# Kernel optimization log

Measured on AMD Instinct MI355X. Metric: run time of the kernel, lower is better.

Reference implementation:

```python
import jax, jax.numpy as jnp
import numpy as np

LN_EPS = 1e-5
NEG_INF = -1e38


def wkv_scan(w, u, k, v):
    """Numerically-stable RWKV WKV recurrence (matches wkv_cuda forward).
    w: [C] (negative decay), u: [C] bonus, k/v: [B,T,C]. Returns y: [B,T,C]."""
    Bdim, T, C = k.shape

    def step(carry, kv_t):
        p, q, o = carry  # running num, den, log-scale, each [B,C]
        kt, vt = kv_t
        no = jnp.maximum(o, u + kt)
        A = jnp.exp(o - no)
        Bw = jnp.exp(u + kt - no)
        y = (A * p + Bw * vt) / (A * q + Bw)
        no2 = jnp.maximum(w + o, kt)
        A2 = jnp.exp(w + o - no2)
        B2 = jnp.exp(kt - no2)
        return (A2 * p + B2 * vt, A2 * q + B2, no2), y

    init = (jnp.zeros((Bdim, C), k.dtype), jnp.zeros((Bdim, C), k.dtype),
            jnp.full((Bdim, C), NEG_INF, k.dtype))
    kT = jnp.moveaxis(k, 1, 0)  # [T,B,C]
    vT = jnp.moveaxis(v, 1, 0)
    _, ys = jax.lax.scan(step, init, (kT, vT))
    return jnp.moveaxis(ys, 0, 1)  # [B,T,C]


def setup_inputs() -> dict:
    key = jax.random.key(0)
    ks = jax.random.split(key, 8)
    B, C, H, W = 16, 192, 56, 56
    s = 0.02
    x = jax.random.normal(ks[0], (B, C, H, W), jnp.float32)
    Wk = jax.random.normal(ks[1], (C, C), jnp.float32) * s
    Wv = jax.random.normal(ks[2], (C, C), jnp.float32) * s
    Wr = jax.random.normal(ks[3], (C, C), jnp.float32) * s
    Wo = jax.random.normal(ks[4], (C, C), jnp.float32) * s
    ln_g = jnp.ones((C,), jnp.float32)
    ln_b = jnp.zeros((C,), jnp.float32)
    w_decay = -6.0 + 0.1 * jax.random.normal(ks[5], (C,), jnp.float32)
    u = 0.1 * jax.random.normal(ks[6], (C,), jnp.float32)
    return {"x": x, "Wk": Wk, "Wv": Wv, "Wr": Wr, "Wo": Wo,
            "ln_g": ln_g, "ln_b": ln_b, "w_decay": w_decay, "u": u}


def reference(x, Wk, Wv, Wr, Wo, ln_g, ln_b, w_decay, u):
    B, C, H, W = x.shape
    xs = jnp.transpose(x.reshape(B, C, H * W), (0, 2, 1))  # [B,T,C]
    k = jnp.einsum('btc,dc->btd', xs, Wk)
    v = jnp.einsum('btc,dc->btd', xs, Wv)
    r = jnp.einsum('btc,dc->btd', xs, Wr)
    real_w = -jnp.exp(w_decay)
    x_fwd = wkv_scan(real_w, u, k, v)
    x_bwd = jnp.flip(wkv_scan(real_w, u, jnp.flip(k, 1), jnp.flip(v, 1)), 1)
    x_bi = 0.5 * (x_fwd + x_bwd)
    h = jax.nn.sigmoid(r) * x_bi
    mu = jnp.mean(h, axis=-1, keepdims=True)
    var = jnp.var(h, axis=-1, keepdims=True)
    h = (h - mu) * jax.lax.rsqrt(var + LN_EPS) * ln_g + ln_b
    out = jnp.einsum('btc,dc->btd', h, Wo)  # dropout is identity at eval
    return jnp.transpose(out, (0, 2, 1)).reshape(B, C, H, W)
```

## Files before the change

kernel.cpp:

```cpp
#include <hip/hip_runtime.h>

#define BB 16
#define CC 192
#define TPIX 3136
#define NCH 49
#define CHL 64
#define NNELE ((size_t)BB * TPIX * CC)
#define NSTATE ((size_t)2 * BB * NCH * CC)
#define WCH (CC * CC)

typedef __attribute__((ext_vector_type(8))) short bf16x8;
typedef __attribute__((ext_vector_type(4))) short bf16x4;
typedef __attribute__((ext_vector_type(4))) float f32x4;
typedef __attribute__((ext_vector_type(16))) float f32x16;

__device__ __forceinline__ unsigned short f2bf(float f) {
    union { float f; unsigned u; } v; v.f = f;
    unsigned r = v.u + 0x7FFFu + ((v.u >> 16) & 1u);
    return (unsigned short)(r >> 16);
}
__device__ __forceinline__ float bf2f(unsigned short h) {
    union { unsigned u; float f; } v; v.u = ((unsigned)h) << 16;
    return v.f;
}


__global__ __launch_bounds__(256) void wcvt_frag(
    const float* __restrict__ Wk, const float* __restrict__ Wv,
    const float* __restrict__ Wr, const float* __restrict__ Wo,
    unsigned short* __restrict__ wfrag)
{
    const int id = blockIdx.x * 256 + threadIdx.x;
    const int m = id / 4608;
    const int r = id % 4608;
    const int tile = r >> 6;
    const int lane = r & 63;
    const int dr = tile / 12, tk = tile % 12;
    const int d = dr * 32 + (lane & 31);
    const int c = tk * 16 + (lane >> 5) * 8;
    const float* W = (m == 0) ? Wk : (m == 1) ? Wv : (m == 2) ? Wr : Wo;
    const float4 a = *(const float4*)&W[d * CC + c];
    const float4 b = *(const float4*)&W[d * CC + c + 4];
    bf16x8 o;
    o[0] = (short)f2bf(a.x); o[1] = (short)f2bf(a.y);
    o[2] = (short)f2bf(a.z); o[3] = (short)f2bf(a.w);
    o[4] = (short)f2bf(b.x); o[5] = (short)f2bf(b.y);
    o[6] = (short)f2bf(b.z); o[7] = (short)f2bf(b.w);
    *(bf16x8*)&wfrag[(size_t)m * WCH + (size_t)tile * 512 + lane * 8] = o;
}

__global__ __launch_bounds__(256) void xcvt_frag(
    const float* __restrict__ x, unsigned short* __restrict__ xfrag)
{
    const int t0 = blockIdx.x * 32;
    const int b  = blockIdx.y;
    __shared__ float ls[CC][33];
    const int tid = threadIdx.x;
#pragma unroll
    for (int it = 0; it < 6; ++it) {
        const int c  = it * 32 + (tid >> 3);
        const int t4 = (tid & 7) * 4;
        *(float4*)&ls[c][t4] =
            *(const float4*)&x[((size_t)b * CC + c) * TPIX + t0 + t4];
    }
    __syncthreads();
    const size_t tbase = ((size_t)(b * TPIX + t0) >> 5) * 12;
#pragma unroll
    for (int it = 0; it < 3; ++it) {
        const int id = it * 256 + tid;
        const int tk = id >> 6;
        const int lane = id & 63;
        const int r32 = lane & 31;
        const int c0 = tk * 16 + (lane >> 5) * 8;
        bf16x8 o;
#pragma unroll
        for (int e = 0; e < 8; ++e)
            o[e] = (short)f2bf(ls[c0 + e][r32]);
        *(bf16x8*)&xfrag[(tbase + tk) * 512 + lane * 8] = o;
    }
}

__global__ __launch_bounds__(512) void proj_mfma32(
    const unsigned short* __restrict__ xfrag,
    const unsigned short* __restrict__ wfrag,
    unsigned short* __restrict__ kbf, unsigned short* __restrict__ vbf,
    unsigned short* __restrict__ rbf)
{
    __shared__ unsigned short wlds[WCH];
    const int tid  = threadIdx.x;
    const int lane = tid & 63;
    const int wv   = tid >> 6;
    const int tw   = wv >> 1;
    const int dwav = wv & 1;
    const int l31  = lane & 31;
    const int kh   = lane >> 5;
    const int m    = blockIdx.z;

    const unsigned short* wm = wfrag + (size_t)m * WCH;
#pragma unroll
    for (int it = 0; it < 9; ++it) {
        const int off = (it * 512 + tid) * 8;
        *(bf16x8*)&wlds[off] = *(const bf16x8*)&wm[off];
    }
    __syncthreads();

    const size_t row0 = (size_t)blockIdx.x * 128 + tw * 32;
    const size_t xtb  = (row0 >> 5) * 12;

    f32x16 acc[3];
#pragma unroll
    for (int nn = 0; nn < 3; ++nn)
#pragma unroll
        for (int e = 0; e < 16; ++e) acc[nn][e] = 0.f;

    bf16x8 xf = *(const bf16x8*)&xfrag[xtb * 512 + lane * 8];
#pragma unroll
    for (int ks = 0; ks < 12; ++ks) {
        bf16x8 nxf;
        if (ks < 11)
            nxf = *(const bf16x8*)&xfrag[(xtb + ks + 1) * 512 + lane * 8];
        bf16x8 wf[3];
#pragma unroll
        for (int nn = 0; nn < 3; ++nn)
            wf[nn] = *(const bf16x8*)&wlds[((dwav * 3 + nn) * 12 + ks) * 512 + lane * 8];
#pragma unroll
        for (int nn = 0; nn < 3; ++nn)
            acc[nn] = __builtin_amdgcn_mfma_f32_32x32x16_bf16(
                xf, wf[nn], acc[nn], 0, 0, 0);
        if (ks < 11) xf = nxf;
    }

    unsigned short* om = (m == 0) ? kbf : (m == 1) ? vbf : rbf;
#pragma unroll
    for (int nn = 0; nn < 3; ++nn) {
        const int d = dwav * 96 + nn * 32 + l31;
#pragma unroll
        for (int q = 0; q < 16; ++q) {
            const int t = (q & 3) + 8 * (q >> 2) + 4 * kh;
            om[(row0 + t) * CC + d] = f2bf(acc[nn][q]);
        }
    }
}

__global__ __launch_bounds__(512) void outproj_mfma32(
    const unsigned short* __restrict__ hfrag,
    const unsigned short* __restrict__ wo,
    float* __restrict__ out)
{
    __shared__ unsigned short wlds[WCH];
    const int tid  = threadIdx.x;
    const int lane = tid & 63;
    const int wv   = tid >> 6;
    const int tw   = wv >> 1;
    const int dwav = wv & 1;
    const int l31  = lane & 31;
    const int kh   = lane >> 5;

#pragma unroll
    for (int it = 0; it < 9; ++it) {
        const int off = (it * 512 + tid) * 8;
        *(bf16x8*)&wlds[off] = *(const bf16x8*)&wo[off];
    }
    __syncthreads();

    const size_t row0 = (size_t)blockIdx.x * 128 + tw * 32;
    const size_t htb  = (row0 >> 5) * 12;

    f32x16 acc[3];
#pragma unroll
    for (int nn = 0; nn < 3; ++nn)
#pragma unroll
        for (int e = 0; e < 16; ++e) acc[nn][e] = 0.f;

    bf16x8 hf = *(const bf16x8*)&hfrag[htb * 512 + lane * 8];
#pragma unroll
    for (int ks = 0; ks < 12; ++ks) {
        bf16x8 nhf;
        if (ks < 11)
            nhf = *(const bf16x8*)&hfrag[(htb + ks + 1) * 512 + lane * 8];
        bf16x8 wf[3];
#pragma unroll
        for (int nn = 0; nn < 3; ++nn)
            wf[nn] = *(const bf16x8*)&wlds[((dwav * 3 + nn) * 12 + ks) * 512 + lane * 8];
#pragma unroll
        for (int nn = 0; nn < 3; ++nn)
            acc[nn] = __builtin_amdgcn_mfma_f32_32x32x16_bf16(
                hf, wf[nn], acc[nn], 0, 0, 0);
        if (ks < 11) hf = nhf;
    }

#pragma unroll
    for (int nn = 0; nn < 3; ++nn) {
        const int d = dwav * 96 + nn * 32 + l31;
#pragma unroll
        for (int q2 = 0; q2 < 4; ++q2) {
            const size_t grow = row0 + 4 * kh + 8 * q2;
            const int b  = (int)(grow / TPIX);
            const int tl = (int)(grow % TPIX);
            f32x4 v4 = {acc[nn][q2 * 4 + 0], acc[nn][q2 * 4 + 1],
                        acc[nn][q2 * 4 + 2], acc[nn][q2 * 4 + 3]};
            *(f32x4*)&out[((size_t)b * CC + d) * TPIX + tl] = v4;
        }
    }
}

__global__ __launch_bounds__(256) void wkv_chunk_kernel(
    const unsigned short* __restrict__ kb, const unsigned short* __restrict__ vb,
    const float* __restrict__ wdec,
    float* __restrict__ sp, float* __restrict__ sq, float* __restrict__ so)
{
    const int gid = blockIdx.x * 256 + threadIdx.x;
    const int c  = gid % CC;
    const int r  = gid / CC;
    const int ch = r % NCH;
    const int r2 = r / NCH;
    const int b  = r2 % BB;
    const int dir = r2 / BB;

    const float w = -__expf(wdec[c]);
    const int tstart = dir ? (TPIX - 1 - ch * CHL) : (ch * CHL);
    const long stride = dir ? -(long)CC : (long)CC;
    long idx = ((long)b * TPIX + tstart) * CC + c;

    float p = 0.f, q = 0.f, o = -1e38f;
#pragma unroll 4
    for (int j = 0; j < CHL; ++j) {
        const float kt = bf2f(kb[idx]), vt = bf2f(vb[idx]);
        const float wo  = w + o;
        const float no2 = fmaxf(wo, kt);
        const float A2  = __expf(wo - no2);
        const float B2  = __expf(kt - no2);
        p = A2 * p + B2 * vt;
        q = A2 * q + B2;
        o = no2;
        idx += stride;
    }
    sp[gid] = p; sq[gid] = q; so[gid] = o;
}

__global__ __launch_bounds__(256) void wkv_prefix_kernel(
    float* __restrict__ sp, float* __restrict__ sq, float* __restrict__ so,
    const float* __restrict__ wdec)
{
    const int tid = blockIdx.x * 256 + threadIdx.x;
    if (tid >= 2 * BB * CC) return;
    const int c = tid % CC;
    const int g = tid / CC;
    const float w  = -__expf(wdec[c]);
    const float wL = w * CHL;

    float P = 0.f, Q = 0.f, O = -1e38f;
    size_t idx = (size_t)g * NCH * CC + c;
    for (int ch = 0; ch < NCH; ++ch) {
        const float pl = sp[idx], ql = sq[idx], ol = so[idx];
        sp[idx] = P; sq[idx] = Q; so[idx] = O;
        const float Ow = O + wL;
        const float no = fmaxf(Ow, ol);
        const float A  = __expf(Ow - no);
        const float Bf = __expf(ol - no);
        P = A * P + Bf * pl;
        Q = A * Q + Bf * ql;
        O = no;
        idx += CC;
    }
}

__global__ __launch_bounds__(256) void wkv_emit_kernel(
    const unsigned short* __restrict__ kb, const unsigned short* __restrict__ vb,
    const float* __restrict__ wdec, const float* __restrict__ ubias,
    const float* __restrict__ sp, const float* __restrict__ sq,
    const float* __restrict__ so,
    unsigned short* __restrict__ yfwd, unsigned short* __restrict__ ybwd)
{
    const int gid = blockIdx.x * 256 + threadIdx.x;
    const int c  = gid % CC;
    const int r  = gid / CC;
    const int ch = r % NCH;
    const int r2 = r / NCH;
    const int b  = r2 % BB;
    const int dir = r2 / BB;

    const float w = -__expf(wdec[c]);
    const float u = ubias[c];
    const int tstart = dir ? (TPIX - 1 - ch * CHL) : (ch * CHL);
    const long stride = dir ? -(long)CC : (long)CC;
    long idx = ((long)b * TPIX + tstart) * CC + c;
    unsigned short* yout = dir ? ybwd : yfwd;

    float p = sp[gid], q = sq[gid], o = so[gid];
#pragma unroll 2
    for (int j = 0; j < CHL; ++j) {
        const float kt = bf2f(kb[idx]), vt = bf2f(vb[idx]);
        const float uk  = u + kt;
        const float no  = fmaxf(o, uk);
        const float A   = __expf(o - no);
        const float Bw  = __expf(uk - no);
        const float num = A * p + Bw * vt;
        const float den = A * q + Bw;
        yout[idx] = f2bf(0.5f * __fdividef(num, den));
        const float wo  = w + o;
        const float no2 = fmaxf(wo, kt);
        const float A2  = __expf(wo - no2);
        const float B2  = __expf(kt - no2);
        p = A2 * p + B2 * vt;
        q = A2 * q + B2;
        o = no2;
        idx += stride;
    }
}

__global__ __launch_bounds__(192) void ln_kernel(
    const unsigned short* __restrict__ rbf,
    const unsigned short* __restrict__ yfwd, const unsigned short* __restrict__ ybwd,
    const float* __restrict__ gamma, const float* __restrict__ beta,
    unsigned short* __restrict__ hfrag)
{
    const size_t row = blockIdx.x;
    const int c = threadIdx.x;
    const size_t idx = row * CC + c;
    const float rv = bf2f(rbf[idx]);
    const float xb = bf2f(yfwd[idx]) + bf2f(ybwd[idx]);
    const float hv = xb / (1.f + __expf(-rv));
    float s = hv, s2 = hv * hv;
#pragma unroll
    for (int off = 1; off < 64; off <<= 1) {
        s  += __shfl_xor(s, off);
        s2 += __shfl_xor(s2, off);
    }
    __shared__ float red[2][3];
    const int wv = threadIdx.x >> 6;
    if ((threadIdx.x & 63) == 0) { red[0][wv] = s; red[1][wv] = s2; }
    __syncthreads();
    s  = red[0][0] + red[0][1] + red[0][2];
    s2 = red[1][0] + red[1][1] + red[1][2];
    const float mu   = s * (1.f / CC);
    const float var  = s2 * (1.f / CC) - mu * mu;
    const float rstd = rsqrtf(var + 1e-5f);
    const float hval = (hv - mu) * rstd * gamma[c] + beta[c];
    const size_t off = ((row >> 5) * 12 + (c >> 4)) * 512 +
                       ((row & 31) + ((c >> 3) & 1) * 32) * 8 + (c & 7);
    hfrag[off] = f2bf(hval);
}

extern "C" void kernel_launch(void* const* d_in, const int* in_sizes, int n_in,
                              void* d_out, int out_size, void* d_ws, size_t ws_size,
                              hipStream_t stream)
{
    const float* x    = (const float*)d_in[0];
    const float* Wk   = (const float*)d_in[1];
    const float* Wv   = (const float*)d_in[2];
    const float* Wr   = (const float*)d_in[3];
    const float* Wo   = (const float*)d_in[4];
    const float* ln_g = (const float*)d_in[5];
    const float* ln_b = (const float*)d_in[6];
    const float* wdec = (const float*)d_in[7];
    const float* u    = (const float*)d_in[8];

    unsigned short* kbf   = (unsigned short*)d_ws;
    unsigned short* vbf   = kbf + NNELE;
    unsigned short* rbf   = vbf + NNELE;
    unsigned short* xfrag = rbf + NNELE;
    unsigned short* wfrag = xfrag + NNELE;
    float* sp = (float*)xfrag;
    float* sq = sp + NSTATE;
    float* so = sq + NSTATE;
    unsigned short* hfrag = kbf;
    unsigned short* yfwd  = (unsigned short*)d_out;
    unsigned short* ybwd  = yfwd + NNELE;
    float* out = (float*)d_out;

    wcvt_frag<<<72, 256, 0, stream>>>(Wk, Wv, Wr, Wo, wfrag);
    xcvt_frag<<<dim3(TPIX / 32, BB), 256, 0, stream>>>(x, xfrag);

    proj_mfma32<<<dim3((BB * TPIX) / 128, 1, 3), 512, 0, stream>>>(
        xfrag, wfrag, kbf, vbf, rbf);

    const int nth = (int)NSTATE;
    wkv_chunk_kernel<<<nth / 256, 256, 0, stream>>>(kbf, vbf, wdec, sp, sq, so);
    wkv_prefix_kernel<<<(2 * BB * CC + 255) / 256, 256, 0, stream>>>(sp, sq, so, wdec);
    wkv_emit_kernel<<<nth / 256, 256, 0, stream>>>(kbf, vbf, wdec, u, sp, sq, so, yfwd, ybwd);

    ln_kernel<<<BB * TPIX, 192, 0, stream>>>(rbf, yfwd, ybwd, ln_g, ln_b, hfrag);

    outproj_mfma32<<<(BB * TPIX) / 128, 512, 0, stream>>>(hfrag, wfrag + 3 * WCH, out);
}
```

Before: 140.1 us.

## Fuse bidirectional WKV emit with sigmoid gating and LayerNorm via LDS tile

```diff
diff --git a/kernel.cpp b/kernel.cpp
--- a/kernel.cpp
+++ b/kernel.cpp
@@ -265,81 +265,100 @@
     }
 }
 
-__global__ __launch_bounds__(256) void wkv_emit_kernel(
+__global__ __launch_bounds__(192) void wkv_emit_ln(
     const unsigned short* __restrict__ kb, const unsigned short* __restrict__ vb,
+    const unsigned short* __restrict__ rbf,
     const float* __restrict__ wdec, const float* __restrict__ ubias,
     const float* __restrict__ sp, const float* __restrict__ sq,
     const float* __restrict__ so,
-    unsigned short* __restrict__ yfwd, unsigned short* __restrict__ ybwd)
-{
-    const int gid = blockIdx.x * 256 + threadIdx.x;
-    const int c  = gid % CC;
-    const int r  = gid / CC;
-    const int ch = r % NCH;
-    const int r2 = r / NCH;
-    const int b  = r2 % BB;
-    const int dir = r2 / BB;
-
+    const float* __restrict__ gamma, const float* __restrict__ beta,
+    unsigned short* __restrict__ hfrag)
+{
+    __shared__ float ylds[CHL][CC + 1];
+    __shared__ float red[2][3][CHL];
+    const int c  = threadIdx.x;
+    const int ch = blockIdx.x;
+    const int b  = blockIdx.y;
     const float w = -__expf(wdec[c]);
     const float u = ubias[c];
-    const int tstart = dir ? (TPIX - 1 - ch * CHL) : (ch * CHL);
-    const long stride = dir ? -(long)CC : (long)CC;
-    long idx = ((long)b * TPIX + tstart) * CC + c;
-    unsigned short* yout = dir ? ybwd : yfwd;
-
-    float p = sp[gid], q = sq[gid], o = so[gid];
-#pragma unroll 2
+    const long rowbase = (long)b * TPIX + (long)ch * CHL;
+
+    {
+        const int gid = (b * NCH + ch) * CC + c;
+        float p = sp[gid], q = sq[gid], o = so[gid];
+        long idx = rowbase * CC + c;
+        for (int j = 0; j < CHL; ++j) {
+            const float kt = bf2f(kb[idx]), vt = bf2f(vb[idx]);
+            const float uk  = u + kt;
+            const float no  = fmaxf(o, uk);
+            const float A   = __expf(o - no);
+            const float Bw  = __expf(uk - no);
+            ylds[j][c] = 0.5f * __fdividef(A * p + Bw * vt, A * q + Bw);
+            const float wo  = w + o;
+            const float no2 = fmaxf(wo, kt);
+            const float A2  = __expf(wo - no2);
+            const float B2  = __expf(kt - no2);
+            p = A2 * p + B2 * vt;
+            q = A2 * q + B2;
+            o = no2;
+            idx += CC;
+        }
+    }
+    {
+        const int gid = ((BB + b) * NCH + (NCH - 1 - ch)) * CC + c;
+        float p = sp[gid], q = sq[gid], o = so[gid];
+        long idx = (rowbase + CHL - 1) * CC + c;
+        for (int j = 0; j < CHL; ++j) {
+            const float kt = bf2f(kb[idx]), vt = bf2f(vb[idx]);
+            const float uk  = u + kt;
+            const float no  = fmaxf(o, uk);
+            const float A   = __expf(o - no);
+            const float Bw  = __expf(uk - no);
+            ylds[CHL - 1 - j][c] += 0.5f * __fdividef(A * p + Bw * vt, A * q + Bw);
+            const float wo  = w + o;
+            const float no2 = fmaxf(wo, kt);
+            const float A2  = __expf(wo - no2);
+            const float B2  = __expf(kt - no2);
+            p = A2 * p + B2 * vt;
+            q = A2 * q + B2;
+            o = no2;
+            idx -= CC;
+        }
+    }
+    {
+        long idx = rowbase * CC + c;
+        for (int j = 0; j < CHL; ++j) {
+            const float rv = bf2f(rbf[idx]);
+            ylds[j][c] *= __frcp_rn(1.f + __expf(-rv));
+            idx += CC;
+        }
+    }
+    __syncthreads();
+    {
+        const int rr = threadIdx.x & 63;
+        const int g  = threadIdx.x >> 6;
+        float s = 0.f, s2 = 0.f;
+#pragma unroll 8
+        for (int i = 0; i < 64; ++i) {
+            const float v = ylds[rr][g * 64 + i];
+            s += v; s2 += v * v;
+        }
+        red[0][g][rr] = s; red[1][g][rr] = s2;
+    }
+    __syncthreads();
+    const float gm = gamma[c], bt = beta[c];
     for (int j = 0; j < CHL; ++j) {
-        const float kt = bf2f(kb[idx]), vt = bf2f(vb[idx]);
-        const float uk  = u + kt;
-        const float no  = fmaxf(o, uk);
-        const float A   = __expf(o - no);
-        const float Bw  = __expf(uk - no);
-        const float num = A * p + Bw * vt;
-        const float den = A * q + Bw;
-        yout[idx] = f2bf(0.5f * __fdividef(num, den));
-        const float wo  = w + o;
-        const float no2 = fmaxf(wo, kt);
-        const float A2  = __expf(wo - no2);
-        const float B2  = __expf(kt - no2);
-        p = A2 * p + B2 * vt;
-        q = A2 * q + B2;
-        o = no2;
-        idx += stride;
-    }
-}
-
-__global__ __launch_bounds__(192) void ln_kernel(
-    const unsigned short* __restrict__ rbf,
-    const unsigned short* __restrict__ yfwd, const unsigned short* __restrict__ ybwd,
-    const float* __restrict__ gamma, const float* __restrict__ beta,
-    unsigned short* __restrict__ hfrag)
-{
-    const size_t row = blockIdx.x;
-    const int c = threadIdx.x;
-    const size_t idx = row * CC + c;
-    const float rv = bf2f(rbf[idx]);
-    const float xb = bf2f(yfwd[idx]) + bf2f(ybwd[idx]);
-    const float hv = xb / (1.f + __expf(-rv));
-    float s = hv, s2 = hv * hv;
-#pragma unroll
-    for (int off = 1; off < 64; off <<= 1) {
-        s  += __shfl_xor(s, off);
-        s2 += __shfl_xor(s2, off);
-    }
-    __shared__ float red[2][3];
-    const int wv = threadIdx.x >> 6;
-    if ((threadIdx.x & 63) == 0) { red[0][wv] = s; red[1][wv] = s2; }
-    __syncthreads();
-    s  = red[0][0] + red[0][1] + red[0][2];
-    s2 = red[1][0] + red[1][1] + red[1][2];
-    const float mu   = s * (1.f / CC);
-    const float var  = s2 * (1.f / CC) - mu * mu;
-    const float rstd = rsqrtf(var + 1e-5f);
-    const float hval = (hv - mu) * rstd * gamma[c] + beta[c];
-    const size_t off = ((row >> 5) * 12 + (c >> 4)) * 512 +
-                       ((row & 31) + ((c >> 3) & 1) * 32) * 8 + (c & 7);
-    hfrag[off] = f2bf(hval);
+        const float s  = red[0][0][j] + red[0][1][j] + red[0][2][j];
+        const float s2 = red[1][0][j] + red[1][1][j] + red[1][2][j];
+        const float mu   = s * (1.f / CC);
+        const float var  = s2 * (1.f / CC) - mu * mu;
+        const float rstd = rsqrtf(var + 1e-5f);
+        const float hval = (ylds[j][c] - mu) * rstd * gm + bt;
+        const size_t row = (size_t)rowbase + j;
+        const size_t off = ((row >> 5) * 12 + (c >> 4)) * 512 +
+                           ((row & 31) + ((c >> 3) & 1) * 32) * 8 + (c & 7);
+        hfrag[off] = f2bf(hval);
+    }
 }
 
 extern "C" void kernel_launch(void* const* d_in, const int* in_sizes, int n_in,
@@ -361,12 +380,10 @@
     unsigned short* rbf   = vbf + NNELE;
     unsigned short* xfrag = rbf + NNELE;
     unsigned short* wfrag = xfrag + NNELE;
+    unsigned short* hfrag = wfrag + 4 * WCH;
     float* sp = (float*)xfrag;
     float* sq = sp + NSTATE;
     float* so = sq + NSTATE;
-    unsigned short* hfrag = kbf;
-    unsigned short* yfwd  = (unsigned short*)d_out;
-    unsigned short* ybwd  = yfwd + NNELE;
     float* out = (float*)d_out;
 
     wcvt_frag<<<72, 256, 0, stream>>>(Wk, Wv, Wr, Wo, wfrag);
@@ -378,9 +395,9 @@
     const int nth = (int)NSTATE;
     wkv_chunk_kernel<<<nth / 256, 256, 0, stream>>>(kbf, vbf, wdec, sp, sq, so);
     wkv_prefix_kernel<<<(2 * BB * CC + 255) / 256, 256, 0, stream>>>(sp, sq, so, wdec);
-    wkv_emit_kernel<<<nth / 256, 256, 0, stream>>>(kbf, vbf, wdec, u, sp, sq, so, yfwd, ybwd);
-
-    ln_kernel<<<BB * TPIX, 192, 0, stream>>>(rbf, yfwd, ybwd, ln_g, ln_b, hfrag);
+
+    wkv_emit_ln<<<dim3(NCH, BB), 192, 0, stream>>>(
+        kbf, vbf, rbf, wdec, u, sp, sq, so, ln_g, ln_b, hfrag);
 
     outproj_mfma32<<<(BB * TPIX) / 128, 512, 0, stream>>>(hfrag, wfrag + 3 * WCH, out);
 }
```

After: 158.5 us. 13.1% more time.
